# Performance work log

Hardware: AMD Instinct MI355X
Metric: run time of the kernel (lower is better)

Reference implementation:

```python
import jax, jax.numpy as jnp
import numpy as np

SR = 22050
FL = 1024      # window_samples
FP = 256       # step_samples
FCEIL = 10000  # formant ceiling (Hz)
MAXF = 4       # max formants
AP_ORDER = 10
R_ORDER = 30
FMIN, FMAX = 50, 500
DK_ITERS = 60  # Durand-Kerner iterations (replaces companion-matrix eig; differentiable)

_w = np.blackman(FL)
WIN = jnp.asarray(_w / np.sqrt(np.sum(_w ** 2)), jnp.float32)  # power-normalized blackman (diffsptk default)


def _frame(x):
    # center-padded framing, frames = T//FP + 1
    pad = FL // 2
    xp = jnp.pad(x, ((0, 0), (pad, pad)))
    n_frames = x.shape[-1] // FP + 1
    idx = jnp.arange(n_frames)[:, None] * FP + jnp.arange(FL)[None, :]
    return xp[:, idx]  # [B, F, FL]


def _levinson(r, order):
    # Levinson-Durbin on autocorrelation r[..., :order+1].
    # Returns (allpole poly coeffs a[..., order+1] with a0=1, reflection coeffs k[..., order]).
    a = jnp.zeros(r.shape[:-1] + (order + 1,), r.dtype).at[..., 0].set(1.0)
    E = r[..., 0]
    ks = []
    for m in range(1, order + 1):
        if m == 1:
            acc = r[..., 1]
        else:
            acc = r[..., m] + jnp.sum(a[..., 1:m] * r[..., m - 1:0:-1], axis=-1)
        k = -acc / (E + 1e-9)
        a_prev = a
        a = a.at[..., m].set(k)
        if m > 1:
            a = a.at[..., 1:m].add(k[..., None] * a_prev[..., m - 1:0:-1])
        E = E * (1.0 - k * k)
        ks.append(k)
    return a, jnp.stack(ks, axis=-1)


def _poly_roots(coeffs):
    # Durand-Kerner simultaneous root iteration, vectorized over frames.
    n = coeffs.shape[-1] - 1
    c = (coeffs / coeffs[..., :1]).astype(jnp.complex64)
    z0 = (0.4 + 0.9j) ** jnp.arange(1, n + 1)
    z = jnp.broadcast_to(z0, c.shape[:-1] + (n,)).astype(jnp.complex64)
    eye = jnp.eye(n, dtype=jnp.complex64)
    def step(z, _):
        p = jnp.zeros_like(z)
        for i in range(n + 1):  # Horner eval of poly at all current root estimates
            p = p * z + c[..., i:i + 1]
        diff = z[..., :, None] - z[..., None, :] + eye
        z = z - p / (jnp.prod(diff, axis=-1) + 1e-12)
        return z, None
    z, _ = jax.lax.scan(step, z, None, length=DK_ITERS)
    return z  # [..., n]


def _root_to_formant(roots):
    # downsampled spectrum covers 0..FCEIL/2, so freq = angle/(2*pi)*FCEIL
    ang = jnp.angle(roots)
    freq = ang / (2.0 * jnp.pi) * FCEIL
    freq = jnp.where(ang > 1e-4, freq, FCEIL * 0.5)  # keep upper-half-plane roots only
    return jnp.sort(freq, axis=-1)[..., :MAXF]  # [B, F, MAXF]


def _pitch(x):
    # autocorrelation pitch tracker
    xf = _frame(x)
    spec = jnp.fft.rfft(xf)
    ac = jnp.fft.irfft(spec * jnp.conj(spec))
    lag_min, lag_max = SR // FMAX, SR // FMIN  # 44..441
    seg = ac[..., lag_min:lag_max + 1]
    peak = jnp.max(seg, axis=-1)
    idx = jnp.argmax(seg, axis=-1)
    nccf = peak / (ac[..., 0] + 1e-9)
    pitch = SR / (lag_min + idx).astype(jnp.float32)
    voicing = (nccf > 0.3).astype(jnp.float32)
    return pitch, voicing, nccf


def _forward(x):
    xf = _frame(x)                 # [B, F, FL]
    xw = xf * WIN
    spec = jnp.fft.rfft(xw)        # [B, F, 513]
    nb = spec.shape[-1]
    ds = int(FCEIL / SR * nb)      # 232 bins -> Nyquist FCEIL/2
    x_ds = spec[..., :ds]
    ac_ds = jnp.fft.irfft(x_ds * jnp.conj(x_ds))   # [B, F, 462]
    ac_us = jnp.fft.irfft(spec * jnp.conj(spec))   # [B, F, 1024]
    ap_env, _ = _levinson(ac_ds, AP_ORDER)
    _, r_coeff_ref = _levinson(ac_us, R_ORDER)
    roots = _poly_roots(ap_env)
    formants = _root_to_formant(roots)
    energy = 10.0 * jnp.log10(jnp.sum(xf * xf, axis=-1) + 1e-10)
    mag = jnp.abs(jnp.fft.rfft(xf))
    freqs = jnp.arange(nb, dtype=jnp.float32) * (SR / FL)
    centroid = jnp.sum(mag * freqs, axis=-1) / (jnp.sum(mag, axis=-1) + 1e-10)
    tilt = ac_ds[..., 1] / (ac_ds[..., 0] + 1e-10)
    pitch, voicing, nccf = _pitch(x)
    pitch = jnp.log(pitch)
    return (formants, energy, centroid, tilt, pitch, voicing, r_coeff_ref, x_ds, nccf)


def setup_inputs() -> dict:
    key = jax.random.key(0)
    x = jax.random.normal(key, (8, 661500), jnp.float32)
    return {"x": x}


def reference(x):
    return _forward(x)
```

## Files before the change

### kernel.cpp

```cpp
#include <hip/hip_runtime.h>
#include <math.h>

#define NSAMP   661500
#define NFRAME  2584
#define NFTOT   20672
#define FPB     6
#define NBLK    3446

#define EN_OFF    82688
#define CEN_OFF   103360
#define TILT_OFF  124032
#define PITCH_OFF 144704
#define VOI_OFF   165376
#define RC_OFF    186048
#define XDS_OFF   806208

__device__ __forceinline__ float waveReduceSum(float v) {
  #pragma unroll
  for (int m = 1; m < 64; m <<= 1) v += __shfl_xor(v, m, 64);
  return v;
}

__device__ __forceinline__ float blockReduceSum(float v, float* s) {
  v = waveReduceSum(v);
  const int w = threadIdx.x >> 6;
  if ((threadIdx.x & 63) == 0) s[w] = v;
  __syncthreads();
  v = s[0] + s[1] + s[2] + s[3];
  __syncthreads();
  return v;
}

__device__ __forceinline__ void fft1024p(float2* X, float2* Y, const float2* tw, int tid) {
  int m = 1;
  #pragma unroll
  for (int s = 0; s < 5; ++s) {
    const int k  = tid & (m - 1);
    const int jm = tid - k;
    const float2 a0 = X[tid];
    const float2 a1 = X[tid + 256];
    const float2 a2 = X[tid + 512];
    const float2 a3 = X[tid + 768];
    const float2 w1 = tw[jm];
    float2 sA, dA, sB, dB;
    sA.x = a0.x + a2.x; sA.y = a0.y + a2.y;
    { const float dx = a0.x - a2.x, dy = a0.y - a2.y;
      dA.x = dx * w1.x + dy * w1.y;
      dA.y = dy * w1.x - dx * w1.y; }
    sB.x = a1.x + a3.x; sB.y = a1.y + a3.y;
    { const float dx = a1.x - a3.x, dy = a1.y - a3.y;
      const float wx = -w1.y, wy = w1.x;
      dB.x = dx * wx + dy * wy;
      dB.y = dy * wx - dx * wy; }
    const float w2x = w1.x * w1.x - w1.y * w1.y;
    const float w2y = 2.0f * w1.x * w1.y;
    const int B = 4 * tid - 3 * k;
    { float2 o;
      o.x = sA.x + sB.x; o.y = sA.y + sB.y;
      Y[B] = o;
      const float dx = sA.x - sB.x, dy = sA.y - sB.y;
      o.x = dx * w2x + dy * w2y;
      o.y = dy * w2x - dx * w2y;
      Y[B + 2 * m] = o; }
    { float2 o;
      o.x = dA.x + dB.x; o.y = dA.y + dB.y;
      Y[B + m] = o;
      const float dx = dA.x - dB.x, dy = dA.y - dB.y;
      o.x = dx * w2x + dy * w2y;
      o.y = dy * w2x - dx * w2y;
      Y[B + 3 * m] = o; }
    __syncthreads();
    float2* tmp = X; X = Y; Y = tmp;
    m <<= 2;
  }
}

template<int ORDER>
__device__ __forceinline__ void levinson_d(const double* r, double* a) {
  double E = r[0];
  a[0] = 1.0;
  #pragma unroll
  for (int m = 1; m <= ORDER; ++m) {
    double acc = r[m];
    #pragma unroll
    for (int i = 1; i < m; ++i) acc += a[i] * r[m - i];
    const double kk = -acc / (E + 1e-9);
    #pragma unroll
    for (int i = 1; i <= (m - 1) / 2; ++i) {
      const double t1 = a[i], t2 = a[m - i];
      a[i]     = t1 + kk * t2;
      a[m - i] = t2 + kk * t1;
    }
    if ((m & 1) == 0) { const double t = a[m >> 1]; a[m >> 1] = t + kk * t; }
    a[m] = kk;
    E *= (1.0 - kk * kk);
  }
}

__device__ __forceinline__ void levinson_f30(const float* r, float* gk) {
  float a[31];
  float E = r[0];
  a[0] = 1.0f;
  #pragma unroll
  for (int m = 1; m <= 30; ++m) {
    float acc = r[m];
    #pragma unroll
    for (int i = 1; i < m; ++i) acc += a[i] * r[m - i];
    const float kk = -acc / (E + 1e-9f);
    #pragma unroll
    for (int i = 1; i <= (m - 1) / 2; ++i) {
      const float t1 = a[i], t2 = a[m - i];
      a[i]     = t1 + kk * t2;
      a[m - i] = t2 + kk * t1;
    }
    if ((m & 1) == 0) { const float t = a[m >> 1]; a[m >> 1] = t + kk * t; }
    a[m] = kk;
    E *= (1.0f - kk * kk);
    if (gk) gk[m - 1] = kk;
  }
}

__device__ __forceinline__ void tail_group(const float* st, float* out,
                                           int frame, int ri, int gbase, bool act) {
  levinson_f30(st, (ri == 0 && act) ? (out + RC_OFF + (size_t)frame * 30)
                                    : (float*)nullptr);

  double rds[11], a10[11];
  #pragma unroll
  for (int l = 0; l < 11; ++l) rds[l] = (double)st[31 + l];
  levinson_d<10>(rds, a10);

  double zr = 0.4, zi = 0.9;
  for (int q = 0; q < ri; ++q) {
    const double nr = zr * 0.4 - zi * 0.9;
    zi = zr * 0.9 + zi * 0.4;
    zr = nr;
  }
  #pragma unroll 1
  for (int it = 0; it < 60; ++it) {
    double ozr[10], ozi[10];
    #pragma unroll
    for (int j = 0; j < 10; ++j) {
      ozr[j] = __shfl(zr, gbase + j, 64);
      ozi[j] = __shfl(zi, gbase + j, 64);
    }
    double pr = 1.0, pi = 0.0;
    #pragma unroll
    for (int q = 1; q <= 10; ++q) {
      const double nr = pr * zr - pi * zi + a10[q];
      pi = pr * zi + pi * zr;
      pr = nr;
    }
    double dr = 1.0, di = 0.0;
    #pragma unroll
    for (int j = 0; j < 10; ++j) {
      const double er = (j == ri) ? 1.0 : (zr - ozr[j]);
      const double ei = (j == ri) ? 0.0 : (zi - ozi[j]);
      const double nr = dr * er - di * ei;
      di = dr * ei + di * er;
      dr = nr;
    }
    dr += 1e-12;
    const double inv = 1.0 / (dr * dr + di * di);
    const double qr = (pr * dr + pi * di) * inv;
    const double qi = (pi * dr - pr * di) * inv;
    zr -= qr;
    zi -= qi;
  }
  const double ang = atan2(zi, zr);
  double freq = (ang > 0.0001) ? (ang / 6.283185307179586476925287 * 10000.0) : 5000.0;
  if (ri >= 10) freq = 1.0e300;

  double f[10];
  #pragma unroll
  for (int j = 0; j < 10; ++j) f[j] = __shfl(freq, gbase + j, 64);
  bool used[10];
  #pragma unroll
  for (int j = 0; j < 10; ++j) used[j] = false;
  float o4[4];
  #pragma unroll
  for (int p2 = 0; p2 < 4; ++p2) {
    double mn = 1.0e300;
    int mj = -1;
    #pragma unroll
    for (int j = 0; j < 10; ++j)
      if (!used[j] && f[j] < mn) { mn = f[j]; mj = j; }
    if (mj >= 0) used[mj] = true;
    o4[p2] = (float)mn;
  }
  if (ri == 0 && act) {
    out[(size_t)frame * 4 + 0] = o4[0];
    out[(size_t)frame * 4 + 1] = o4[1];
    out[(size_t)frame * 4 + 2] = o4[2];
    out[(size_t)frame * 4 + 3] = o4[3];
  }
}

__global__ void __launch_bounds__(256, 8)
feat_front(const float* __restrict__ x, float* __restrict__ out,
           float* __restrict__ ws, const int xds_pf, const int nccf_off) {
  __shared__ float2 A[1024];
  __shared__ float2 Bb[1024];
  __shared__ float2 tw[256];
  __shared__ float  sred[12];
  __shared__ int    sredi[4];
  __shared__ float  aprt[4][11];

  const int tid   = threadIdx.x;
  const int w     = tid >> 6;
  const int lane  = tid & 63;
  const int fbase = blockIdx.x * FPB;
  const int np    = (fbase + FPB <= NFTOT) ? FPB : (NFTOT - fbase);

  {
    const float th = (float)tid * (6.2831853071795864769f / 1024.0f);
    float sn, cn;
    sincosf(th, &sn, &cn);
    tw[tid] = make_float2(cn, sn);
  }
  float wv[4];
  float wsq = 0.0f;
  #pragma unroll
  for (int q = 0; q < 4; ++q) {
    const int n = tid + q * 256;
    const float th = (float)n * (6.2831853071795864769f / 1023.0f);
    const float wn = 0.42f - 0.5f * cosf(th) + 0.08f * cosf(2.0f * th);
    wv[q] = wn;
    wsq += wn * wn;
  }
  float ctab[11];
  #pragma unroll
  for (int l = 0; l < 11; ++l)
    ctab[l] = cosf((float)(tid * l) * (6.2831853071795864769f / 462.0f));
  const float wgt462 = ((tid == 0 || tid == 231) ? 1.0f : 2.0f) * (1.0f / 462.0f);
  __syncthreads();
  const float invn = 1.0f / sqrtf(blockReduceSum(wsq, sred));

  #pragma unroll 1
  for (int p = 0; p < np; ++p) {
    const int fg = fbase + p;
    const int bb = fg / NFRAME;
    const int fr = fg - bb * NFRAME;
    const float* xb = x + (size_t)bb * NSAMP;

    #pragma unroll
    for (int q = 0; q < 4; ++q) {
      const int n = tid + q * 256;
      const int g = fr * 256 + n - 512;
      const float xv = (g >= 0 && g < NSAMP) ? xb[g] : 0.0f;
      A[n] = make_float2(xv * wv[q] * invn, xv);
    }
    __syncthreads();

    fft1024p(A, Bb, tw, tid);

    float cs0 = 0.0f, cs1 = 0.0f;
    float myPw = 0.0f;
    float pw0, pf0, pw1, pf1;
    {
      const int k = tid;
      const float2 Zk = Bb[k];
      const float2 Zn = Bb[(1024 - k) & 1023];
      const float xwr = 0.5f * (Zk.x + Zn.x);
      const float xwi = 0.5f * (Zk.y - Zn.y);
      const float xfr = 0.5f * (Zk.y + Zn.y);
      const float xfi = -0.5f * (Zk.x - Zn.x);
      pw0 = xwr * xwr + xwi * xwi;
      pf0 = xfr * xfr + xfi * xfi;
      const float mg = sqrtf(pf0);
      cs0 += mg;
      cs1 += mg * ((float)k * (22050.0f / 1024.0f));
      if (k < 232) {
        myPw = pw0;
        if (xds_pf == 232) {
          __builtin_nontemporal_store(xwr, &out[XDS_OFF + (size_t)fg * 232 + k]);
        } else {
          float* dst = out + XDS_OFF + ((size_t)fg * 232 + k) * 2;
          __builtin_nontemporal_store(xwr, dst);
          __builtin_nontemporal_store(xwi, dst + 1);
        }
      }
    }
    {
      const int k = tid + 256;
      const float2 Zk = Bb[k];
      const float2 Zn = Bb[1024 - k];
      const float xwr = 0.5f * (Zk.x + Zn.x);
      const float xwi = 0.5f * (Zk.y - Zn.y);
      const float xfr = 0.5f * (Zk.y + Zn.y);
      const float xfi = -0.5f * (Zk.x - Zn.x);
      pw1 = xwr * xwr + xwi * xwi;
      pf1 = xfr * xfr + xfi * xfi;
      const float mg = sqrtf(pf1);
      cs0 += mg;
      cs1 += mg * ((float)k * (22050.0f / 1024.0f));
    }
    if (tid == 0) {
      const int k = 512;
      const float2 Zk = Bb[k];
      const float2 Zn = Bb[512];
      const float xwr = 0.5f * (Zk.x + Zn.x);
      const float xwi = 0.5f * (Zk.y - Zn.y);
      const float xfr = 0.5f * (Zk.y + Zn.y);
      const float xfi = -0.5f * (Zk.x - Zn.x);
      const float pw = xwr * xwr + xwi * xwi;
      const float pf = xfr * xfr + xfi * xfi;
      const float mg = sqrtf(pf);
      cs0 += mg;
      cs1 += mg * ((float)k * (22050.0f / 1024.0f));
      A[512] = make_float2(pw * 1024.0f, pf);
    }

    {
      const float2 v0 = make_float2(pw0 * 1024.0f, pf0);
      const float2 v1 = make_float2(pw1 * 1024.0f, pf1);
      A[tid]       = v0;
      A[tid + 256] = v1;
      if (tid > 0) A[1024 - tid] = v0;
      A[768 - tid] = v1;
    }
    __syncthreads();

    fft1024p(A, Bb, tw, tid);

    float pv = -3.0e38f;
    int   pl = 1 << 30;
    for (int l = 44 + tid; l <= 441; l += 256) {
      const float v = Bb[l].y;
      if (v > pv) { pv = v; pl = l; }
    }
    #pragma unroll
    for (int m = 1; m < 64; m <<= 1) {
      const float ov = __shfl_xor(pv, m, 64);
      const int   ol = __shfl_xor(pl, m, 64);
      if (ov > pv || (ov == pv && ol < pl)) { pv = ov; pl = ol; }
    }
    cs0 = waveReduceSum(cs0);
    cs1 = waveReduceSum(cs1);
    if (lane == 0) { sred[w] = pv; sredi[w] = pl; sred[4 + w] = cs0; sred[8 + w] = cs1; }
    const float pwW = myPw * wgt462;
    #pragma unroll
    for (int l = 0; l < 11; ++l) {
      const float t = waveReduceSum(pwW * ctab[l]);
      if (lane == 0) aprt[w][l] = t;
    }
    __syncthreads();

    if (tid == 0) {
      float bv = sred[0]; int bl = sredi[0];
      #pragma unroll
      for (int q = 1; q < 4; ++q)
        if (sred[q] > bv || (sred[q] == bv && sredi[q] < bl)) { bv = sred[q]; bl = sredi[q]; }
      const float ac0  = Bb[0].y * (1.0f / 1024.0f);
      const float peak = bv * (1.0f / 1024.0f);
      const float nccf = peak / (ac0 + 1e-9f);
      out[PITCH_OFF + fg] = logf(22050.0f / (float)bl);
      out[VOI_OFF + fg]   = (nccf > 0.3f) ? 1.0f : 0.0f;
      out[nccf_off + fg]  = nccf;
      out[EN_OFF + fg]    = 10.0f * log10f(ac0 + 1e-10f);
      const float c0 = sred[4] + sred[5] + sred[6] + sred[7];
      const float c1 = sred[8] + sred[9] + sred[10] + sred[11];
      out[CEN_OFF + fg]   = c1 / (c0 + 1e-10f);
      const float a0 = aprt[0][0] + aprt[1][0] + aprt[2][0] + aprt[3][0];
      const float a1 = aprt[0][1] + aprt[1][1] + aprt[2][1] + aprt[3][1];
      out[TILT_OFF + fg]  = a1 / (a0 + 1e-10f);
    }
    if (tid < 11)
      ws[(size_t)fg * 42 + 31 + tid] =
          aprt[0][tid] + aprt[1][tid] + aprt[2][tid] + aprt[3][tid];
    if (tid < 31)
      ws[(size_t)fg * 42 + tid] = Bb[tid].x * (1.0f / 1048576.0f);
  }
}

__global__ void __launch_bounds__(256)
feat_tail(const float* __restrict__ ws, float* __restrict__ out) {
  const int tid  = threadIdx.x;
  const int w    = tid >> 6;
  const int lane = tid & 63;
  const int g    = lane / 10;
  const int ri   = lane - g * 10;
  const int gbase = g * 10;
  int frame = blockIdx.x * 24 + w * 6 + ((g < 6) ? g : 5);
  const bool act = (g < 6) && (frame < NFTOT);
  if (frame >= NFTOT) frame = NFTOT - 1;

  float st[42];
  #pragma unroll
  for (int j = 0; j < 42; ++j) st[j] = ws[(size_t)frame * 42 + j];

  tail_group(st, out, frame, ri, gbase, act);
}

__global__ void __launch_bounds__(256, 8)
feat_mono_fb(const float* __restrict__ x, float* __restrict__ out,
             const int xds_pf, const int nccf_off) {
  __shared__ float2 A[1024];
  __shared__ float2 Bb[1024];
  __shared__ float2 tw[256];
  __shared__ float  sred[12];
  __shared__ int    sredi[4];
  __shared__ float  stash[FPB][42];
  __shared__ float  aprt[4][11];

  const int tid   = threadIdx.x;
  const int w     = tid >> 6;
  const int lane  = tid & 63;
  const int fbase = blockIdx.x * FPB;
  const int np    = (fbase + FPB <= NFTOT) ? FPB : (NFTOT - fbase);

  {
    const float th = (float)tid * (6.2831853071795864769f / 1024.0f);
    float sn, cn;
    sincosf(th, &sn, &cn);
    tw[tid] = make_float2(cn, sn);
  }
  float wv[4];
  float wsq = 0.0f;
  #pragma unroll
  for (int q = 0; q < 4; ++q) {
    const int n = tid + q * 256;
    const float th = (float)n * (6.2831853071795864769f / 1023.0f);
    const float wn = 0.42f - 0.5f * cosf(th) + 0.08f * cosf(2.0f * th);
    wv[q] = wn;
    wsq += wn * wn;
  }
  float ctab[11];
  #pragma unroll
  for (int l = 0; l < 11; ++l)
    ctab[l] = cosf((float)(tid * l) * (6.2831853071795864769f / 462.0f));
  const float wgt462 = ((tid == 0 || tid == 231) ? 1.0f : 2.0f) * (1.0f / 462.0f);
  __syncthreads();
  const float invn = 1.0f / sqrtf(blockReduceSum(wsq, sred));

  #pragma unroll 1
  for (int p = 0; p < np; ++p) {
    const int fg = fbase + p;
    const int bb = fg / NFRAME;
    const int fr = fg - bb * NFRAME;
    const float* xb = x + (size_t)bb * NSAMP;

    #pragma unroll
    for (int q = 0; q < 4; ++q) {
      const int n = tid + q * 256;
      const int g = fr * 256 + n - 512;
      const float xv = (g >= 0 && g < NSAMP) ? xb[g] : 0.0f;
      A[n] = make_float2(xv * wv[q] * invn, xv);
    }
    __syncthreads();

    fft1024p(A, Bb, tw, tid);

    float cs0 = 0.0f, cs1 = 0.0f;
    float myPw = 0.0f;
    {
      const int k = tid;
      const float2 Zk = Bb[k];
      const float2 Zn = Bb[(1024 - k) & 1023];
      const float xwr = 0.5f * (Zk.x + Zn.x);
      const float xwi = 0.5f * (Zk.y - Zn.y);
      const float xfr = 0.5f * (Zk.y + Zn.y);
      const float xfi = -0.5f * (Zk.x - Zn.x);
      const float pw = xwr * xwr + xwi * xwi;
      const float pf = xfr * xfr + xfi * xfi;
      const float mg = sqrtf(pf);
      cs0 += mg;
      cs1 += mg * ((float)k * (22050.0f / 1024.0f));
      if (k < 232) {
        myPw = pw;
        if (xds_pf == 232) {
          out[XDS_OFF + (size_t)fg * 232 + k] = xwr;
        } else {
          ((float2*)(out + XDS_OFF))[(size_t)fg * 232 + k] = make_float2(xwr, xwi);
        }
      }
    }
    {
      const int k = tid + 256;
      const float2 Zk = Bb[k];
      const float2 Zn = Bb[1024 - k];
      const float xfr = 0.5f * (Zk.y + Zn.y);
      const float xfi = -0.5f * (Zk.x - Zn.x);
      const float pf = xfr * xfr + xfi * xfi;
      const float mg = sqrtf(pf);
      cs0 += mg;
      cs1 += mg * ((float)k * (22050.0f / 1024.0f));
    }
    if (tid == 0) {
      const int k = 512;
      const float2 Zk = Bb[k];
      const float2 Zn = Bb[512];
      const float xfr = 0.5f * (Zk.y + Zn.y);
      const float xfi = -0.5f * (Zk.x - Zn.x);
      const float pf = xfr * xfr + xfi * xfi;
      const float mg = sqrtf(pf);
      cs0 += mg;
      cs1 += mg * ((float)k * (22050.0f / 1024.0f));
    }

    #pragma unroll
    for (int q = 0; q < 4; ++q) {
      const int k2 = tid + q * 256;
      const int km = (k2 <= 512) ? k2 : (1024 - k2);
      const float2 Zk = Bb[km];
      const float2 Zn = Bb[(1024 - km) & 1023];
      const float xwr = 0.5f * (Zk.x + Zn.x);
      const float xwi = 0.5f * (Zk.y - Zn.y);
      const float xfr = 0.5f * (Zk.y + Zn.y);
      const float xfi = -0.5f * (Zk.x - Zn.x);
      const float pw = xwr * xwr + xwi * xwi;
      const float pf = xfr * xfr + xfi * xfi;
      A[k2] = make_float2(pw * 1024.0f, pf);
    }
    __syncthreads();

    fft1024p(A, Bb, tw, tid);

    float pv = -3.0e38f;
    int   pl = 1 << 30;
    for (int l = 44 + tid; l <= 441; l += 256) {
      const float v = Bb[l].y;
      if (v > pv) { pv = v; pl = l; }
    }
    #pragma unroll
    for (int m = 1; m < 64; m <<= 1) {
      const float ov = __shfl_xor(pv, m, 64);
      const int   ol = __shfl_xor(pl, m, 64);
      if (ov > pv || (ov == pv && ol < pl)) { pv = ov; pl = ol; }
    }
    cs0 = waveReduceSum(cs0);
    cs1 = waveReduceSum(cs1);
    if (lane == 0) { sred[w] = pv; sredi[w] = pl; sred[4 + w] = cs0; sred[8 + w] = cs1; }
    const float pwW = myPw * wgt462;
    #pragma unroll
    for (int l = 0; l < 11; ++l) {
      const float t = waveReduceSum(pwW * ctab[l]);
      if (lane == 0) aprt[w][l] = t;
    }
    __syncthreads();

    if (tid == 0) {
      float bv = sred[0]; int bl = sredi[0];
      #pragma unroll
      for (int q = 1; q < 4; ++q)
        if (sred[q] > bv || (sred[q] == bv && sredi[q] < bl)) { bv = sred[q]; bl = sredi[q]; }
      const float ac0  = Bb[0].y * (1.0f / 1024.0f);
      const float peak = bv * (1.0f / 1024.0f);
      const float nccf = peak / (ac0 + 1e-9f);
      out[PITCH_OFF + fg] = logf(22050.0f / (float)bl);
      out[VOI_OFF + fg]   = (nccf > 0.3f) ? 1.0f : 0.0f;
      out[nccf_off + fg]  = nccf;
      out[EN_OFF + fg]    = 10.0f * log10f(ac0 + 1e-10f);
      const float c0 = sred[4] + sred[5] + sred[6] + sred[7];
      const float c1 = sred[8] + sred[9] + sred[10] + sred[11];
      out[CEN_OFF + fg]   = c1 / (c0 + 1e-10f);
      const float a0 = aprt[0][0] + aprt[1][0] + aprt[2][0] + aprt[3][0];
      const float a1 = aprt[0][1] + aprt[1][1] + aprt[2][1] + aprt[3][1];
      out[TILT_OFF + fg]  = a1 / (a0 + 1e-10f);
    }
    if (tid < 11)
      stash[p][31 + tid] = aprt[0][tid] + aprt[1][tid] + aprt[2][tid] + aprt[3][tid];
    if (tid < 31) stash[p][tid] = Bb[tid].x * (1.0f / 1048576.0f);
  }
  __syncthreads();

  if (w == 0) {
    const int g     = lane / 10;
    const int ri    = lane - g * 10;
    const int gbase = g * 10;
    const int gg    = (g < FPB) ? g : (FPB - 1);
    const bool act  = (g < np);
    const int fg    = fbase + gg;
    tail_group(&stash[gg][0], out, fg, ri, gbase, act);
  }
}

extern "C" void kernel_launch(void* const* d_in, const int* in_sizes, int n_in,
                              void* d_out, int out_size, void* d_ws, size_t ws_size,
                              hipStream_t stream) {
  (void)in_sizes; (void)n_in;
  const float* x = (const float*)d_in[0];
  float* out = (float*)d_out;
  int xds_pf = 232;
  if (out_size >= XDS_OFF + NFTOT * 464 + NFTOT) xds_pf = 464;
  const int nccf_off = XDS_OFF + NFTOT * xds_pf;

  const size_t need = (size_t)NFTOT * 42 * 4;
  if (d_ws != nullptr && ws_size >= need) {
    float* ws = (float*)d_ws;
    feat_front<<<dim3(NBLK), dim3(256), 0, stream>>>(x, out, ws, xds_pf, nccf_off);
    feat_tail<<<dim3((NFTOT + 23) / 24), dim3(256), 0, stream>>>(ws, out);
  } else {
    feat_mono_fb<<<dim3(NBLK), dim3(256), 0, stream>>>(x, out, xds_pf, nccf_off);
  }
}
```

Before: 319.0 us.

## Pad FFT shared-memory layout and fuse the first radix-4 stage into the load

Shared-memory FFT buffers are padded with one extra float2 every four entries, to reduce LDS bank conflicts on the strided butterfly writes. The first radix-4 stage now runs in registers right after the global load, which removes one shared-memory round trip and one barrier per FFT. The per-frame front half is factored into a shared helper, and the mono kernel's power-spectrum rebuild now uses the same mirrored scheme as the split kernel. The larger LDS footprint lowers the launch_bounds occupancy hints (to 7 and 6 blocks).

```diff
diff --git a/kernel.cpp b/kernel.cpp
--- a/kernel.cpp
+++ b/kernel.cpp
@@ -15,6 +15,9 @@
 #define RC_OFF    186048
 #define XDS_OFF   806208
 
+#define IDX(i) ((i) + ((i) >> 2))
+#define LSZ 1280
+
 __device__ __forceinline__ float waveReduceSum(float v) {
   #pragma unroll
   for (int m = 1; m < 64; m <<= 1) v += __shfl_xor(v, m, 64);
@@ -31,44 +34,71 @@
   return v;
 }
 
-__device__ __forceinline__ void fft1024p(float2* X, float2* Y, const float2* tw, int tid) {
+__device__ __forceinline__ void fused_bfly(const float2 a0, const float2 a1,
+                                           const float2 a2, const float2 a3,
+                                           const float2 w1, float2* o) {
+  float2 sA, dA, sB, dB;
+  sA.x = a0.x + a2.x; sA.y = a0.y + a2.y;
+  { const float dx = a0.x - a2.x, dy = a0.y - a2.y;
+    dA.x = dx * w1.x + dy * w1.y;
+    dA.y = dy * w1.x - dx * w1.y; }
+  sB.x = a1.x + a3.x; sB.y = a1.y + a3.y;
+  { const float dx = a1.x - a3.x, dy = a1.y - a3.y;
+    const float wx = -w1.y, wy = w1.x;
+    dB.x = dx * wx + dy * wy;
+    dB.y = dy * wx - dx * wy; }
+  const float w2x = w1.x * w1.x - w1.y * w1.y;
+  const float w2y = 2.0f * w1.x * w1.y;
+  o[0].x = sA.x + sB.x; o[0].y = sA.y + sB.y;
+  { const float dx = sA.x - sB.x, dy = sA.y - sB.y;
+    o[2].x = dx * w2x + dy * w2y;
+    o[2].y = dy * w2x - dx * w2y; }
+  o[1].x = dA.x + dB.x; o[1].y = dA.y + dB.y;
+  { const float dx = dA.x - dB.x, dy = dA.y - dB.y;
+    o[3].x = dx * w2x + dy * w2y;
+    o[3].y = dy * w2x - dx * w2y; }
+}
+
+__device__ __forceinline__ void fft4iter(float2* X, float2* Y, const float2* tw, int tid) {
+  int m = 4;
+  #pragma unroll
+  for (int s = 0; s < 4; ++s) {
+    const int k  = tid & (m - 1);
+    const int jm = tid - k;
+    const float2 a0 = X[IDX(tid)];
+    const float2 a1 = X[IDX(tid + 256)];
+    const float2 a2 = X[IDX(tid + 512)];
+    const float2 a3 = X[IDX(tid + 768)];
+    float2 o[4];
+    fused_bfly(a0, a1, a2, a3, tw[jm], o);
+    const int B = 4 * tid - 3 * k;
+    Y[IDX(B)]         = o[0];
+    Y[IDX(B + m)]     = o[1];
+    Y[IDX(B + 2 * m)] = o[2];
+    Y[IDX(B + 3 * m)] = o[3];
+    __syncthreads();
+    float2* tmp = X; X = Y; Y = tmp;
+    m <<= 2;
+  }
+}
+
+__device__ __forceinline__ void fft1024p5(float2* X, float2* Y, const float2* tw, int tid) {
   int m = 1;
   #pragma unroll
   for (int s = 0; s < 5; ++s) {
     const int k  = tid & (m - 1);
     const int jm = tid - k;
-    const float2 a0 = X[tid];
-    const float2 a1 = X[tid + 256];
-    const float2 a2 = X[tid + 512];
-    const float2 a3 = X[tid + 768];
-    const float2 w1 = tw[jm];
-    float2 sA, dA, sB, dB;
-    sA.x = a0.x + a2.x; sA.y = a0.y + a2.y;
-    { const float dx = a0.x - a2.x, dy = a0.y - a2.y;
-      dA.x = dx * w1.x + dy * w1.y;
-      dA.y = dy * w1.x - dx * w1.y; }
-    sB.x = a1.x + a3.x; sB.y = a1.y + a3.y;
-    { const float dx = a1.x - a3.x, dy = a1.y - a3.y;
-      const float wx = -w1.y, wy = w1.x;
-      dB.x = dx * wx + dy * wy;
-      dB.y = dy * wx - dx * wy; }
-    const float w2x = w1.x * w1.x - w1.y * w1.y;
-    const float w2y = 2.0f * w1.x * w1.y;
+    const float2 a0 = X[IDX(tid)];
+    const float2 a1 = X[IDX(tid + 256)];
+    const float2 a2 = X[IDX(tid + 512)];
+    const float2 a3 = X[IDX(tid + 768)];
+    float2 o[4];
+    fused_bfly(a0, a1, a2, a3, tw[jm], o);
     const int B = 4 * tid - 3 * k;
-    { float2 o;
-      o.x = sA.x + sB.x; o.y = sA.y + sB.y;
-      Y[B] = o;
-      const float dx = sA.x - sB.x, dy = sA.y - sB.y;
-      o.x = dx * w2x + dy * w2y;
-      o.y = dy * w2x - dx * w2y;
-      Y[B + 2 * m] = o; }
-    { float2 o;
-      o.x = dA.x + dB.x; o.y = dA.y + dB.y;
-      Y[B + m] = o;
-      const float dx = dA.x - dB.x, dy = dA.y - dB.y;
-      o.x = dx * w2x + dy * w2y;
-      o.y = dy * w2x - dx * w2y;
-      Y[B + 3 * m] = o; }
+    Y[IDX(B)]         = o[0];
+    Y[IDX(B + m)]     = o[1];
+    Y[IDX(B + 2 * m)] = o[2];
+    Y[IDX(B + 3 * m)] = o[3];
     __syncthreads();
     float2* tmp = X; X = Y; Y = tmp;
     m <<= 2;
@@ -196,11 +226,106 @@
   }
 }
 
-__global__ void __launch_bounds__(256, 8)
+__device__ __forceinline__ void front_frame(
+    const float* __restrict__ xb, float* __restrict__ out,
+    float2* A, float2* Bb, const float2* tw, const float2 w1t,
+    const float* wv, float invn, int tid, int fg, int fr, int xds_pf,
+    float& cs0, float& cs1, float& myPw) {
+  {
+    float2 z[4];
+    #pragma unroll
+    for (int q = 0; q < 4; ++q) {
+      const int n = tid + q * 256;
+      const int g = fr * 256 + n - 512;
+      const float xv = (g >= 0 && g < NSAMP) ? xb[g] : 0.0f;
+      z[q] = make_float2(xv * wv[q] * invn, xv);
+    }
+    float2 o[4];
+    fused_bfly(z[0], z[1], z[2], z[3], w1t, o);
+    const int B = 4 * tid;
+    Bb[IDX(B)]     = o[0];
+    Bb[IDX(B + 1)] = o[1];
+    Bb[IDX(B + 2)] = o[2];
+    Bb[IDX(B + 3)] = o[3];
+  }
+  __syncthreads();
+
+  fft4iter(Bb, A, tw, tid);
+
+  cs0 = 0.0f; cs1 = 0.0f; myPw = 0.0f;
+  float pw0, pf0, pw1, pf1;
+  {
+    const int k = tid;
+    const float2 Zk = Bb[IDX(k)];
+    const float2 Zn = Bb[IDX((1024 - k) & 1023)];
+    const float xwr = 0.5f * (Zk.x + Zn.x);
+    const float xwi = 0.5f * (Zk.y - Zn.y);
+    const float xfr = 0.5f * (Zk.y + Zn.y);
+    const float xfi = -0.5f * (Zk.x - Zn.x);
+    pw0 = xwr * xwr + xwi * xwi;
+    pf0 = xfr * xfr + xfi * xfi;
+    const float mg = sqrtf(pf0);
+    cs0 += mg;
+    cs1 += mg * ((float)k * (22050.0f / 1024.0f));
+    if (k < 232) {
+      myPw = pw0;
+      if (xds_pf == 232) {
+        __builtin_nontemporal_store(xwr, &out[XDS_OFF + (size_t)fg * 232 + k]);
+      } else {
+        float* dst = out + XDS_OFF + ((size_t)fg * 232 + k) * 2;
+        __builtin_nontemporal_store(xwr, dst);
+        __builtin_nontemporal_store(xwi, dst + 1);
+      }
+    }
+  }
+  {
+    const int k = tid + 256;
+    const float2 Zk = Bb[IDX(k)];
+    const float2 Zn = Bb[IDX(1024 - k)];
+    const float xwr = 0.5f * (Zk.x + Zn.x);
+    const float xwi = 0.5f * (Zk.y - Zn.y);
+    const float xfr = 0.5f * (Zk.y + Zn.y);
+    const float xfi = -0.5f * (Zk.x - Zn.x);
+    pw1 = xwr * xwr + xwi * xwi;
+    pf1 = xfr * xfr + xfi * xfi;
+    const float mg = sqrtf(pf1);
+    cs0 += mg;
+    cs1 += mg * ((float)k * (22050.0f / 1024.0f));
+  }
+  if (tid == 0) {
+    const int k = 512;
+    const float2 Zk = Bb[IDX(k)];
+    const float2 Zn = Bb[IDX(512)];
+    const float xwr = 0.5f * (Zk.x + Zn.x);
+    const float xwi = 0.5f * (Zk.y - Zn.y);
+    const float xfr = 0.5f * (Zk.y + Zn.y);
+    const float xfi = -0.5f * (Zk.x - Zn.x);
+    const float pw = xwr * xwr + xwi * xwi;
+    const float pf = xfr * xfr + xfi * xfi;
+    const float mg = sqrtf(pf);
+    cs0 += mg;
+    cs1 += mg * ((float)k * (22050.0f / 1024.0f));
+    A[IDX(512)] = make_float2(pw * 1024.0f, pf);
+  }
+
+  {
+    const float2 v0 = make_float2(pw0 * 1024.0f, pf0);
+    const float2 v1 = make_float2(pw1 * 1024.0f, pf1);
+    A[IDX(tid)]       = v0;
+    A[IDX(tid + 256)] = v1;
+    if (tid > 0) A[IDX(1024 - tid)] = v0;
+    A[IDX(768 - tid)] = v1;
+  }
+  __syncthreads();
+
+  fft1024p5(A, Bb, tw, tid);
+}
+
+__global__ void __launch_bounds__(256, 7)
 feat_front(const float* __restrict__ x, float* __restrict__ out,
            float* __restrict__ ws, const int xds_pf, const int nccf_off) {
-  __shared__ float2 A[1024];
-  __shared__ float2 Bb[1024];
+  __shared__ float2 A[LSZ];
+  __shared__ float2 Bb[LSZ];
   __shared__ float2 tw[256];
   __shared__ float  sred[12];
   __shared__ int    sredi[4];
@@ -235,6 +360,7 @@
   const float wgt462 = ((tid == 0 || tid == 231) ? 1.0f : 2.0f) * (1.0f / 462.0f);
   __syncthreads();
   const float invn = 1.0f / sqrtf(blockReduceSum(wsq, sred));
+  const float2 w1t = tw[tid];
 
   #pragma unroll 1
   for (int p = 0; p < np; ++p) {
@@ -243,90 +369,14 @@
     const int fr = fg - bb * NFRAME;
     const float* xb = x + (size_t)bb * NSAMP;
 
-    #pragma unroll
-    for (int q = 0; q < 4; ++q) {
-      const int n = tid + q * 256;
-      const int g = fr * 256 + n - 512;
-      const float xv = (g >= 0 && g < NSAMP) ? xb[g] : 0.0f;
-      A[n] = make_float2(xv * wv[q] * invn, xv);
-    }
-    __syncthreads();
-
-    fft1024p(A, Bb, tw, tid);
-
-    float cs0 = 0.0f, cs1 = 0.0f;
-    float myPw = 0.0f;
-    float pw0, pf0, pw1, pf1;
-    {
-      const int k = tid;
-      const float2 Zk = Bb[k];
-      const float2 Zn = Bb[(1024 - k) & 1023];
-      const float xwr = 0.5f * (Zk.x + Zn.x);
-      const float xwi = 0.5f * (Zk.y - Zn.y);
-      const float xfr = 0.5f * (Zk.y + Zn.y);
-      const float xfi = -0.5f * (Zk.x - Zn.x);
-      pw0 = xwr * xwr + xwi * xwi;
-      pf0 = xfr * xfr + xfi * xfi;
-      const float mg = sqrtf(pf0);
-      cs0 += mg;
-      cs1 += mg * ((float)k * (22050.0f / 1024.0f));
-      if (k < 232) {
-        myPw = pw0;
-        if (xds_pf == 232) {
-          __builtin_nontemporal_store(xwr, &out[XDS_OFF + (size_t)fg * 232 + k]);
-        } else {
-          float* dst = out + XDS_OFF + ((size_t)fg * 232 + k) * 2;
-          __builtin_nontemporal_store(xwr, dst);
-          __builtin_nontemporal_store(xwi, dst + 1);
-        }
-      }
-    }
-    {
-      const int k = tid + 256;
-      const float2 Zk = Bb[k];
-      const float2 Zn = Bb[1024 - k];
-      const float xwr = 0.5f * (Zk.x + Zn.x);
-      const float xwi = 0.5f * (Zk.y - Zn.y);
-      const float xfr = 0.5f * (Zk.y + Zn.y);
-      const float xfi = -0.5f * (Zk.x - Zn.x);
-      pw1 = xwr * xwr + xwi * xwi;
-      pf1 = xfr * xfr + xfi * xfi;
-      const float mg = sqrtf(pf1);
-      cs0 += mg;
-      cs1 += mg * ((float)k * (22050.0f / 1024.0f));
-    }
-    if (tid == 0) {
-      const int k = 512;
-      const float2 Zk = Bb[k];
-      const float2 Zn = Bb[512];
-      const float xwr = 0.5f * (Zk.x + Zn.x);
-      const float xwi = 0.5f * (Zk.y - Zn.y);
-      const float xfr = 0.5f * (Zk.y + Zn.y);
-      const float xfi = -0.5f * (Zk.x - Zn.x);
-      const float pw = xwr * xwr + xwi * xwi;
-      const float pf = xfr * xfr + xfi * xfi;
-      const float mg = sqrtf(pf);
-      cs0 += mg;
-      cs1 += mg * ((float)k * (22050.0f / 1024.0f));
-      A[512] = make_float2(pw * 1024.0f, pf);
-    }
-
-    {
-      const float2 v0 = make_float2(pw0 * 1024.0f, pf0);
-      const float2 v1 = make_float2(pw1 * 1024.0f, pf1);
-      A[tid]       = v0;
-      A[tid + 256] = v1;
-      if (tid > 0) A[1024 - tid] = v0;
-      A[768 - tid] = v1;
-    }
-    __syncthreads();
-
-    fft1024p(A, Bb, tw, tid);
+    float cs0, cs1, myPw;
+    front_frame(xb, out, A, Bb, tw, w1t, wv, invn, tid, fg, fr, xds_pf,
+                cs0, cs1, myPw);
 
     float pv = -3.0e38f;
     int   pl = 1 << 30;
     for (int l = 44 + tid; l <= 441; l += 256) {
-      const float v = Bb[l].y;
+      const float v = Bb[IDX(l)].y;
       if (v > pv) { pv = v; pl = l; }
     }
     #pragma unroll
@@ -351,7 +401,7 @@
       #pragma unroll
       for (int q = 1; q < 4; ++q)
         if (sred[q] > bv || (sred[q] == bv && sredi[q] < bl)) { bv = sred[q]; bl = sredi[q]; }
-      const float ac0  = Bb[0].y * (1.0f / 1024.0f);
+      const float ac0  = Bb[IDX(0)].y * (1.0f / 1024.0f);
       const float peak = bv * (1.0f / 1024.0f);
       const float nccf = peak / (ac0 + 1e-9f);
       out[PITCH_OFF + fg] = logf(22050.0f / (float)bl);
@@ -369,7 +419,7 @@
       ws[(size_t)fg * 42 + 31 + tid] =
           aprt[0][tid] + aprt[1][tid] + aprt[2][tid] + aprt[3][tid];
     if (tid < 31)
-      ws[(size_t)fg * 42 + tid] = Bb[tid].x * (1.0f / 1048576.0f);
+      ws[(size_t)fg * 42 + tid] = Bb[IDX(tid)].x * (1.0f / 1048576.0f);
   }
 }
 
@@ -392,16 +442,16 @@
   tail_group(st, out, frame, ri, gbase, act);
 }
 
-__global__ void __launch_bounds__(256, 8)
+__global__ void __launch_bounds__(256, 6)
 feat_mono_fb(const float* __restrict__ x, float* __restrict__ out,
              const int xds_pf, const int nccf_off) {
-  __shared__ float2 A[1024];
-  __shared__ float2 Bb[1024];
+  __shared__ float2 A[LSZ];
+  __shared__ float2 Bb[LSZ];
   __shared__ float2 tw[256];
   __shared__ float  sred[12];
   __shared__ int    sredi[4];
+  __shared__ float  aprt[4][11];
   __shared__ float  stash[FPB][42];
-  __shared__ float  aprt[4][11];
 
   const int tid   = threadIdx.x;
   const int w     = tid >> 6;
@@ -432,6 +482,7 @@
   const float wgt462 = ((tid == 0 || tid == 231) ? 1.0f : 2.0f) * (1.0f / 462.0f);
   __syncthreads();
   const float invn = 1.0f / sqrtf(blockReduceSum(wsq, sred));
+  const float2 w1t = tw[tid];
 
   #pragma unroll 1
   for (int p = 0; p < np; ++p) {
@@ -440,86 +491,14 @@
     const int fr = fg - bb * NFRAME;
     const float* xb = x + (size_t)bb * NSAMP;
 
-    #pragma unroll
-    for (int q = 0; q < 4; ++q) {
-      const int n = tid + q * 256;
-      const int g = fr * 256 + n - 512;
-      const float xv = (g >= 0 && g < NSAMP) ? xb[g] : 0.0f;
-      A[n] = make_float2(xv * wv[q] * invn, xv);
-    }
-    __syncthreads();
-
-    fft1024p(A, Bb, tw, tid);
-
-    float cs0 = 0.0f, cs1 = 0.0f;
-    float myPw = 0.0f;
-    {
-      const int k = tid;
-      const float2 Zk = Bb[k];
-      const float2 Zn = Bb[(1024 - k) & 1023];
-      const float xwr = 0.5f * (Zk.x + Zn.x);
-      const float xwi = 0.5f * (Zk.y - Zn.y);
-      const float xfr = 0.5f * (Zk.y + Zn.y);
-      const float xfi = -0.5f * (Zk.x - Zn.x);
-      const float pw = xwr * xwr + xwi * xwi;
-      const float pf = xfr * xfr + xfi * xfi;
-      const float mg = sqrtf(pf);
-      cs0 += mg;
-      cs1 += mg * ((float)k * (22050.0f / 1024.0f));
-      if (k < 232) {
-        myPw = pw;
-        if (xds_pf == 232) {
-          out[XDS_OFF + (size_t)fg * 232 + k] = xwr;
-        } else {
-          ((float2*)(out + XDS_OFF))[(size_t)fg * 232 + k] = make_float2(xwr, xwi);
-        }
-      }
-    }
-    {
-      const int k = tid + 256;
-      const float2 Zk = Bb[k];
-      const float2 Zn = Bb[1024 - k];
-      const float xfr = 0.5f * (Zk.y + Zn.y);
-      const float xfi = -0.5f * (Zk.x - Zn.x);
-      const float pf = xfr * xfr + xfi * xfi;
-      const float mg = sqrtf(pf);
-      cs0 += mg;
-      cs1 += mg * ((float)k * (22050.0f / 1024.0f));
-    }
-    if (tid == 0) {
-      const int k = 512;
-      const float2 Zk = Bb[k];
-      const float2 Zn = Bb[512];
-      const float xfr = 0.5f * (Zk.y + Zn.y);
-      const float xfi = -0.5f * (Zk.x - Zn.x);
-      const float pf = xfr * xfr + xfi * xfi;
-      const float mg = sqrtf(pf);
-      cs0 += mg;
-      cs1 += mg * ((float)k * (22050.0f / 1024.0f));
-    }
-
-    #pragma unroll
-    for (int q = 0; q < 4; ++q) {
-      const int k2 = tid + q * 256;
-      const int km = (k2 <= 512) ? k2 : (1024 - k2);
-      const float2 Zk = Bb[km];
-      const float2 Zn = Bb[(1024 - km) & 1023];
-      const float xwr = 0.5f * (Zk.x + Zn.x);
-      const float xwi = 0.5f * (Zk.y - Zn.y);
-      const float xfr = 0.5f * (Zk.y + Zn.y);
-      const float xfi = -0.5f * (Zk.x - Zn.x);
-      const float pw = xwr * xwr + xwi * xwi;
-      const float pf = xfr * xfr + xfi * xfi;
-      A[k2] = make_float2(pw * 1024.0f, pf);
-    }
-    __syncthreads();
-
-    fft1024p(A, Bb, tw, tid);
+    float cs0, cs1, myPw;
+    front_frame(xb, out, A, Bb, tw, w1t, wv, invn, tid, fg, fr, xds_pf,
+                cs0, cs1, myPw);
 
     float pv = -3.0e38f;
     int   pl = 1 << 30;
     for (int l = 44 + tid; l <= 441; l += 256) {
-      const float v = Bb[l].y;
+      const float v = Bb[IDX(l)].y;
       if (v > pv) { pv = v; pl = l; }
     }
     #pragma unroll
@@ -544,7 +523,7 @@
       #pragma unroll
       for (int q = 1; q < 4; ++q)
         if (sred[q] > bv || (sred[q] == bv && sredi[q] < bl)) { bv = sred[q]; bl = sredi[q]; }
-      const float ac0  = Bb[0].y * (1.0f / 1024.0f);
+      const float ac0  = Bb[IDX(0)].y * (1.0f / 1024.0f);
       const float peak = bv * (1.0f / 1024.0f);
       const float nccf = peak / (ac0 + 1e-9f);
       out[PITCH_OFF + fg] = logf(22050.0f / (float)bl);
@@ -560,7 +539,7 @@
     }
     if (tid < 11)
       stash[p][31 + tid] = aprt[0][tid] + aprt[1][tid] + aprt[2][tid] + aprt[3][tid];
-    if (tid < 31) stash[p][tid] = Bb[tid].x * (1.0f / 1048576.0f);
+    if (tid < 31) stash[p][tid] = Bb[IDX(tid)].x * (1.0f / 1048576.0f);
   }
   __syncthreads();
 
```

Result: slower. 339.6 us (+6.5%).
